# Performance work log

Hardware: AMD Instinct MI355X
Metric: run time of the kernel (lower is better)

## Reference

```python
import jax, jax.numpy as jnp
import numpy as np

N_NODES = 50000
N_EDGES = 800000
D_FEAT = 64      # num_src_feats == num_dst_feats
D_EDGE = 16      # num_edge_feats
D_HID = 16       # hidden width of both tiny MLPs
D_MSG = 64       # msg_size
D_OUT = 64       # num_out_feats


def setup_inputs() -> dict:
    key = jax.random.key(0)
    ks = jax.random.split(key, 12)
    x = jax.random.normal(ks[0], (N_NODES, D_FEAT), dtype=jnp.float32)
    edge_feats = jax.random.normal(ks[1], (N_EDGES, D_EDGE), dtype=jnp.float32)
    src = jax.random.randint(ks[2], (N_EDGES,), 0, N_NODES, dtype=jnp.int32)
    dst = jax.random.randint(ks[3], (N_EDGES,), 0, N_NODES, dtype=jnp.int32)

    def linear_params(k, fan_in, fan_out):
        kw, kb = jax.random.split(k)
        bound = 1.0 / np.sqrt(fan_in)
        W = jax.random.uniform(kw, (fan_in, fan_out), jnp.float32, -bound, bound)
        b = jax.random.uniform(kb, (fan_out,), jnp.float32, -bound, bound)
        return W, b

    # fc_msg: [D_EDGE + D_FEAT, 16, D_MSG]
    msg_W1, msg_b1 = linear_params(ks[4], D_EDGE + D_FEAT, D_HID)
    msg_W2, msg_b2 = linear_params(ks[5], D_HID, D_MSG)
    # fc_udt: [D_FEAT + D_MSG, 16, D_OUT]
    udt_W1, udt_b1 = linear_params(ks[6], D_FEAT + D_MSG, D_HID)
    udt_W2, udt_b2 = linear_params(ks[7], D_HID, D_OUT)

    return {
        "x": x, "edge_feats": edge_feats, "src": src, "dst": dst,
        "msg_W1": msg_W1, "msg_b1": msg_b1, "msg_W2": msg_W2, "msg_b2": msg_b2,
        "udt_W1": udt_W1, "udt_b1": udt_b1, "udt_W2": udt_W2, "udt_b2": udt_b2,
    }


def reference(x, edge_feats, src, dst,
              msg_W1, msg_b1, msg_W2, msg_b2,
              udt_W1, udt_b1, udt_W2, udt_b2):
    # message: m_e = MLP([edge_feats_e, x[src_e]])   (cat order: edge first)
    edge_in = jnp.concatenate([edge_feats, x[src]], axis=1)  # [E, D_EDGE+D_FEAT]
    h = jax.nn.relu(edge_in @ msg_W1 + msg_b1)
    m = h @ msg_W2 + msg_b2  # [E, D_MSG]

    # reduce: r_v = max over incoming edges (DGL fills 0 for nodes w/o in-edges)
    r = jax.ops.segment_max(m, dst, num_segments=N_NODES)  # [N, D_MSG]
    r = jnp.where(jnp.isfinite(r), r, 0.0)

    # update: out_v = MLP([x_v, r_v])
    upd_in = jnp.concatenate([x, r], axis=1)  # [N, D_FEAT+D_MSG]
    h2 = jax.nn.relu(upd_in @ udt_W1 + udt_b1)
    return h2 @ udt_W2 + udt_b2  # [N, D_OUT]
```

## Files before the change

kernel.cpp:

```cpp
#include <hip/hip_runtime.h>

#define N_NODES 50000
#define N_EDGES 800000

#define NB  196
#define PB  128
#define EPB 6250
#define PITERS 25
#define CAP 7680

__device__ __forceinline__ unsigned fkey(float f) {
    unsigned u = __float_as_uint(f);
    return (u & 0x80000000u) ? ~u : (u | 0x80000000u);
}
#define KEY_NEG_INF 0x007FFFFFu

__device__ __forceinline__ void wave_lds_fence() {
    asm volatile("s_waitcnt lgkmcnt(0)" ::: "memory");
    __builtin_amdgcn_sched_barrier(0);
}

__global__ __launch_bounds__(256) void chist_kernel(const int* __restrict__ dst,
                                                    unsigned* __restrict__ bcnt) {
    __shared__ unsigned lh[NB];
    const int t = threadIdx.x, b = blockIdx.x;
    if (t < NB) lh[t] = 0u;
    __syncthreads();
    const int e0 = b * EPB;
#pragma unroll
    for (int it = 0; it < PITERS; ++it) {
        const int i = it * 256 + t;
        if (i < EPB) atomicAdd(&lh[(unsigned)dst[e0 + i] >> 8], 1u);
    }
    __syncthreads();
    if (t < NB) bcnt[b * NB + t] = lh[t];
}

__global__ __launch_bounds__(256) void cscan_kernel(const unsigned* __restrict__ bcnt,
                                                    unsigned* __restrict__ gstart,
                                                    unsigned* __restrict__ boffG,
                                                    unsigned* __restrict__ totG) {
    __shared__ unsigned wsum[4];
    const int t = threadIdx.x, lane = t & 63, w = t >> 6;
    unsigned tot = 0;
    if (t < NB)
        for (int k = 0; k < PB; ++k) tot += bcnt[k * NB + t];
    unsigned v = (t < NB) ? tot : 0u;
    const unsigned orig = v;
#pragma unroll
    for (int d = 1; d < 64; d <<= 1) {
        unsigned n = __shfl_up(v, d, 64);
        if (lane >= d) v += n;
    }
    if (lane == 63) wsum[w] = v;
    __syncthreads();
    unsigned woff = 0;
#pragma unroll
    for (int i = 0; i < 3; ++i) if (i < w) woff += wsum[i];
    const unsigned boff = woff + v - orig;
    if (t < NB) {
        boffG[t] = boff;
        totG[t]  = tot;
        unsigned run = boff;
        for (int k = 0; k < PB; ++k) { gstart[k * NB + t] = run; run += bcnt[k * NB + t]; }
    }
}

__global__ __launch_bounds__(256) void partition_kernel(const int* __restrict__ dst,
                                                        const unsigned* __restrict__ gstart,
                                                        unsigned long long* __restrict__ part) {
    __shared__ unsigned long long st[EPB];
    __shared__ unsigned lh[NB], lstart[NB], lc[NB], gs[NB];
    __shared__ unsigned wsum[4];
    const int t = threadIdx.x, b = blockIdx.x, lane = t & 63, w = t >> 6;
    if (t < NB) { lh[t] = 0u; gs[t] = gstart[b * NB + t]; }
    __syncthreads();
    const int e0 = b * EPB;
#pragma unroll
    for (int it = 0; it < PITERS; ++it) {
        const int i = it * 256 + t;
        if (i < EPB) atomicAdd(&lh[(unsigned)dst[e0 + i] >> 8], 1u);
    }
    __syncthreads();
    {
        unsigned v = (t < NB) ? lh[t] : 0u;
        const unsigned orig = v;
#pragma unroll
        for (int d = 1; d < 64; d <<= 1) {
            unsigned n = __shfl_up(v, d, 64);
            if (lane >= d) v += n;
        }
        if (lane == 63) wsum[w] = v;
        __syncthreads();
        unsigned woff = 0;
#pragma unroll
        for (int i = 0; i < 3; ++i) if (i < w) woff += wsum[i];
        if (t < NB) { lstart[t] = woff + v - orig; lc[t] = woff + v - orig; }
    }
    __syncthreads();
#pragma unroll
    for (int it = 0; it < PITERS; ++it) {
        const int i = it * 256 + t;
        if (i < EPB) {
            const int e = e0 + i;
            const unsigned d = (unsigned)dst[e];
            const unsigned p = atomicAdd(&lc[d >> 8], 1u);
            st[p] = ((unsigned long long)d << 32) | (unsigned)e;
        }
    }
    __syncthreads();
#pragma unroll
    for (int it = 0; it < PITERS; ++it) {
        const int i = it * 256 + t;
        if (i < EPB) {
            const unsigned long long pv = st[i];
            const unsigned bkt = (unsigned)(pv >> 40);
            part[gs[bkt] + ((unsigned)i - lstart[bkt])] = pv;
        }
    }
}

__global__ __launch_bounds__(256) void finesort_kernel(const unsigned long long* __restrict__ part,
                                                       const unsigned* __restrict__ boffG,
                                                       const unsigned* __restrict__ totG,
                                                       unsigned long long* __restrict__ dsf) {
    __shared__ unsigned long long st[CAP];
    __shared__ unsigned fh[256], fstart[256];
    __shared__ unsigned wsum[4];
    const int t = threadIdx.x, b = blockIdx.x, lane = t & 63, w = t >> 6;
    const unsigned base = boffG[b], cnt = totG[b];
    fh[t] = 0u;
    __syncthreads();
    const int iters = (int)((cnt + 255u) >> 8);
    for (int it = 0; it < iters; ++it) {
        const unsigned i = (unsigned)it * 256u + (unsigned)t;
        if (i < cnt) atomicAdd(&fh[(unsigned)(part[base + i] >> 32) & 255u], 1u);
    }
    __syncthreads();
    {
        unsigned v = fh[t];
        const unsigned orig = v;
#pragma unroll
        for (int d = 1; d < 64; d <<= 1) {
            unsigned n = __shfl_up(v, d, 64);
            if (lane >= d) v += n;
        }
        if (lane == 63) wsum[w] = v;
        __syncthreads();
        unsigned woff = 0;
#pragma unroll
        for (int i = 0; i < 3; ++i) if (i < w) woff += wsum[i];
        fstart[t] = woff + v - orig;
    }
    __syncthreads();
    if (cnt <= CAP) {
        for (int it = 0; it < iters; ++it) {
            const unsigned i = (unsigned)it * 256u + (unsigned)t;
            if (i < cnt) {
                const unsigned long long pv = part[base + i];
                const unsigned p = atomicAdd(&fstart[(unsigned)(pv >> 32) & 255u], 1u);
                st[p] = pv;
            }
        }
        __syncthreads();
        for (int it = 0; it < iters; ++it) {
            const unsigned i = (unsigned)it * 256u + (unsigned)t;
            if (i < cnt) dsf[base + i] = st[i];
        }
    } else {
        for (int it = 0; it < iters; ++it) {
            const unsigned i = (unsigned)it * 256u + (unsigned)t;
            if (i < cnt) {
                const unsigned long long pv = part[base + i];
                const unsigned p = atomicAdd(&fstart[(unsigned)(pv >> 32) & 255u], 1u);
                dsf[base + p] = pv;
            }
        }
    }
}

__global__ __launch_bounds__(256) void init_kernel(
    unsigned* __restrict__ rkey,
    const float* __restrict__ x, const float* __restrict__ W1,
    const float* __restrict__ b1, float* __restrict__ xw)
{
    const int i = blockIdx.x * 256 + threadIdx.x;
    reinterpret_cast<uint4*>(rkey)[i] =
        make_uint4(KEY_NEG_INF, KEY_NEG_INF, KEY_NEG_INF, KEY_NEG_INF);
    if (i < N_NODES) {
        float acc[16];
#pragma unroll
        for (int k = 0; k < 16; ++k) acc[k] = b1[k];
        const float4* xp = reinterpret_cast<const float4*>(x) + (size_t)i * 16;
#pragma unroll
        for (int c = 0; c < 16; ++c) {
            float4 tv = xp[c];
            const float xv[4] = {tv.x, tv.y, tv.z, tv.w};
#pragma unroll
            for (int q = 0; q < 4; ++q) {
                const int row = 16 + 4 * c + q;
#pragma unroll
                for (int k = 0; k < 16; ++k)
                    acc[k] = fmaf(xv[q], W1[row * 16 + k], acc[k]);
            }
        }
        float4* op = reinterpret_cast<float4*>(xw) + (size_t)i * 4;
#pragma unroll
        for (int c = 0; c < 4; ++c) {
            float4 o; o.x = acc[4*c]; o.y = acc[4*c+1]; o.z = acc[4*c+2]; o.w = acc[4*c+3];
            op[c] = o;
        }
    }
}

__global__ __launch_bounds__(256) void init0_kernel(unsigned* __restrict__ rkey) {
    const int i = blockIdx.x * 256 + threadIdx.x;
    reinterpret_cast<uint4*>(rkey)[i] =
        make_uint4(KEY_NEG_INF, KEY_NEG_INF, KEY_NEG_INF, KEY_NEG_INF);
}

__global__ __launch_bounds__(256) void edge_csr2_kernel(
    const float* __restrict__ xw, const float* __restrict__ ef,
    const int* __restrict__ src,
    const unsigned long long* __restrict__ ds,
    const float* __restrict__ W1, const float* __restrict__ W2,
    const float* __restrict__ b2,
    unsigned* __restrict__ rkey)
{
    const int lane = threadIdx.x & 63;
    const int w    = threadIdx.x >> 6;
    const int wave = blockIdx.x * 4 + w;
    const int base = wave * 64;
    const int slot = base + lane;

    __shared__ unsigned mld[4][64][17];
    __shared__ int      dldA[4][66];
    int* dld = &dldA[w][1];

    const unsigned long long pv = ds[slot];
    const int e = (int)(unsigned)pv;
    const int d = (int)(pv >> 32);
    dld[lane] = d;
    if (lane == 0)  dld[-1] = (base == 0) ? -1 : (int)(ds[base - 1] >> 32);
    if (lane == 63) dld[64] = (base + 64 >= N_EDGES) ? -1 : (int)(ds[base + 64] >> 32);

    float in[16];
    const float4* efp = reinterpret_cast<const float4*>(ef) + (size_t)e * 4;
#pragma unroll
    for (int c = 0; c < 4; ++c) {
        float4 tv = efp[c];
        in[4*c+0]=tv.x; in[4*c+1]=tv.y; in[4*c+2]=tv.z; in[4*c+3]=tv.w;
    }
    const int s = src[e];
    float h[16];
    const float4* xp = reinterpret_cast<const float4*>(xw) + (size_t)s * 4;
#pragma unroll
    for (int c = 0; c < 4; ++c) {
        float4 tv = xp[c];
        h[4*c+0]=tv.x; h[4*c+1]=tv.y; h[4*c+2]=tv.z; h[4*c+3]=tv.w;
    }
#pragma unroll
    for (int i = 0; i < 16; ++i)
#pragma unroll
        for (int k = 0; k < 16; ++k)
            h[k] = fmaf(in[i], W1[i*16 + k], h[k]);
#pragma unroll
    for (int k = 0; k < 16; ++k) h[k] = fmaxf(h[k], 0.0f);

    const int q  = lane >> 4;
    const int jj = lane & 15;

#pragma unroll
    for (int j0 = 0; j0 < 64; j0 += 16) {
        float m[16];
#pragma unroll
        for (int t = 0; t < 16; ++t) m[t] = b2[j0 + t];
#pragma unroll
        for (int k = 0; k < 16; ++k)
#pragma unroll
            for (int t = 0; t < 16; ++t)
                m[t] = fmaf(h[k], W2[k*64 + j0 + t], m[t]);

        wave_lds_fence();
#pragma unroll
        for (int t = 0; t < 16; ++t) mld[w][lane][t] = fkey(m[t]);
        wave_lds_fence();

        const int s0 = q * 16;
        unsigned run = KEY_NEG_INF;
        int  dprev = dld[s0 - 1];
        bool phead = (dld[s0] != dprev);
        dprev = dld[s0];
        run = mld[w][s0][jj];
#pragma unroll
        for (int i = 1; i < 16; ++i) {
            const int ss = s0 + i;
            const int dsv = dld[ss];
            if (dsv != dprev) {
                unsigned* addr = &rkey[((size_t)dprev << 6) + (unsigned)(j0 + jj)];
                if (phead) *addr = run;
                else       atomicMax(addr, run);
                run = KEY_NEG_INF;
                phead = true;
            }
            run = max(run, mld[w][ss][jj]);
            dprev = dsv;
        }
        const bool ptail = (dld[s0 + 16] != dprev);
        unsigned* addr = &rkey[((size_t)dprev << 6) + (unsigned)(j0 + jj)];
        if (phead && ptail) *addr = run;
        else                atomicMax(addr, run);
    }
}

__global__ __launch_bounds__(256) void node_kernel(
    const float* __restrict__ x, const unsigned* rkey,
    const float* __restrict__ W1, const float* __restrict__ b1,
    const float* __restrict__ W2, const float* __restrict__ b2,
    float* out)
{
    const int v = blockIdx.x * 256 + threadIdx.x;
    if (v >= N_NODES) return;

    float in[128];
    const float4* xp = reinterpret_cast<const float4*>(x) + (size_t)v * 16;
#pragma unroll
    for (int c = 0; c < 16; ++c) {
        float4 tv = xp[c];
        in[4*c+0]=tv.x; in[4*c+1]=tv.y; in[4*c+2]=tv.z; in[4*c+3]=tv.w;
    }
    const uint4* rp = reinterpret_cast<const uint4*>(rkey) + (size_t)v * 16;
#pragma unroll
    for (int c = 0; c < 16; ++c) {
        uint4 tv = rp[c];
        unsigned ks[4] = {tv.x, tv.y, tv.z, tv.w};
#pragma unroll
        for (int qq = 0; qq < 4; ++qq) {
            unsigned k = ks[qq];
            unsigned u = (k & 0x80000000u) ? (k ^ 0x80000000u) : ~k;
            float f = __uint_as_float(u);
            if (!(f >= -3.402823466e38f && f <= 3.402823466e38f)) f = 0.0f;
            in[64 + 4*c + qq] = f;
        }
    }

    float h[16];
#pragma unroll
    for (int k = 0; k < 16; ++k) h[k] = b1[k];
#pragma unroll
    for (int i = 0; i < 128; ++i)
#pragma unroll
        for (int k = 0; k < 16; ++k)
            h[k] = fmaf(in[i], W1[i*16 + k], h[k]);
#pragma unroll
    for (int k = 0; k < 16; ++k) h[k] = fmaxf(h[k], 0.0f);

    float* op = out + (size_t)v * 64;
#pragma unroll
    for (int c = 0; c < 16; ++c) {
        float oo[4];
#pragma unroll
        for (int qq = 0; qq < 4; ++qq) {
            float a = b2[4*c + qq];
#pragma unroll
            for (int k = 0; k < 16; ++k)
                a = fmaf(h[k], W2[k*64 + 4*c + qq], a);
            oo[qq] = a;
        }
        float4 o; o.x=oo[0]; o.y=oo[1]; o.z=oo[2]; o.w=oo[3];
        reinterpret_cast<float4*>(op)[c] = o;
    }
}

__global__ __launch_bounds__(64) void edge_kernel(
    const float* __restrict__ x, const float* __restrict__ ef,
    const int* __restrict__ src, const int* __restrict__ dst,
    const float* __restrict__ W1, const float* __restrict__ b1,
    const float* __restrict__ W2, const float* __restrict__ b2,
    unsigned* __restrict__ rkey)
{
    const int lane = threadIdx.x;
    const int e    = blockIdx.x * 64 + lane;

    __shared__ unsigned mld[64][17];
    __shared__ int      dld[64];

    float in[80];
    const float4* efp = reinterpret_cast<const float4*>(ef) + (size_t)e * 4;
#pragma unroll
    for (int c = 0; c < 4; ++c) {
        float4 tv = efp[c];
        in[4*c+0]=tv.x; in[4*c+1]=tv.y; in[4*c+2]=tv.z; in[4*c+3]=tv.w;
    }
    const int s = src[e];
    dld[lane] = dst[e];
    const float4* xp = reinterpret_cast<const float4*>(x) + (size_t)s * 16;
#pragma unroll
    for (int c = 0; c < 16; ++c) {
        float4 tv = xp[c];
        in[16+4*c+0]=tv.x; in[16+4*c+1]=tv.y; in[16+4*c+2]=tv.z; in[16+4*c+3]=tv.w;
    }

    float h[16];
#pragma unroll
    for (int k = 0; k < 16; ++k) h[k] = b1[k];
#pragma unroll
    for (int i = 0; i < 80; ++i)
#pragma unroll
        for (int k = 0; k < 16; ++k)
            h[k] = fmaf(in[i], W1[i*16 + k], h[k]);
#pragma unroll
    for (int k = 0; k < 16; ++k) h[k] = fmaxf(h[k], 0.0f);

    const int er = lane >> 4;
    const int jj = lane & 15;

#pragma unroll
    for (int j0 = 0; j0 < 64; j0 += 16) {
        float m[16];
#pragma unroll
        for (int t = 0; t < 16; ++t) m[t] = b2[j0 + t];
#pragma unroll
        for (int k = 0; k < 16; ++k)
#pragma unroll
            for (int t = 0; t < 16; ++t)
                m[t] = fmaf(h[k], W2[k*64 + j0 + t], m[t]);

        wave_lds_fence();
#pragma unroll
        for (int t = 0; t < 16; ++t) mld[lane][t] = fkey(m[t]);
        wave_lds_fence();

#pragma unroll
        for (int eg = 0; eg < 16; ++eg) {
            const int ee = (eg << 2) | er;
            atomicMax(&rkey[((size_t)dld[ee] << 6) + (unsigned)(j0 + jj)],
                      mld[ee][jj]);
        }
    }
}

extern "C" void kernel_launch(void* const* d_in, const int* in_sizes, int n_in,
                              void* d_out, int out_size, void* d_ws, size_t ws_size,
                              hipStream_t stream) {
    const float* x   = (const float*)d_in[0];
    const float* ef  = (const float*)d_in[1];
    const int*   src = (const int*)d_in[2];
    const int*   dst = (const int*)d_in[3];
    const float* mW1 = (const float*)d_in[4];
    const float* mb1 = (const float*)d_in[5];
    const float* mW2 = (const float*)d_in[6];
    const float* mb2 = (const float*)d_in[7];
    const float* uW1 = (const float*)d_in[8];
    const float* ub1 = (const float*)d_in[9];
    const float* uW2 = (const float*)d_in[10];
    const float* ub2 = (const float*)d_in[11];

    unsigned* rkey = (unsigned*)d_out;
    float*    out  = (float*)d_out;

    const size_t WS_NEEDED = (size_t)N_EDGES * 8
                           + (size_t)(PB * NB * 2 + 512 + N_EDGES) * 4;

    if (ws_size >= WS_NEEDED) {
        unsigned long long* dsf = (unsigned long long*)d_ws;
        unsigned* bcnt   = (unsigned*)(dsf + N_EDGES);
        unsigned* gstart = bcnt + PB * NB;
        unsigned* boffG  = gstart + PB * NB;
        unsigned* totG   = boffG + 256;
        float*    xw     = (float*)(totG + 256);
        unsigned long long* part = (unsigned long long*)d_out;

        hipLaunchKernelGGL(chist_kernel,     dim3(PB),   dim3(256), 0, stream, dst, bcnt);
        hipLaunchKernelGGL(cscan_kernel,     dim3(1),    dim3(256), 0, stream, bcnt, gstart, boffG, totG);
        hipLaunchKernelGGL(partition_kernel, dim3(PB),   dim3(256), 0, stream, dst, gstart, part);
        hipLaunchKernelGGL(finesort_kernel,  dim3(NB),   dim3(256), 0, stream, part, boffG, totG, dsf);
        hipLaunchKernelGGL(init_kernel,      dim3(3125), dim3(256), 0, stream, rkey, x, mW1, mb1, xw);
        hipLaunchKernelGGL(edge_csr2_kernel, dim3(3125), dim3(256), 0, stream,
                           xw, ef, src, dsf, mW1, mW2, mb2, rkey);
    } else {
        hipLaunchKernelGGL(init0_kernel, dim3(3125), dim3(256), 0, stream, rkey);
        hipLaunchKernelGGL(edge_kernel, dim3(12500), dim3(64), 0, stream,
                           x, ef, src, dst, mW1, mb1, mW2, mb2, rkey);
    }

    hipLaunchKernelGGL(node_kernel, dim3((N_NODES + 255) / 256), dim3(256), 0, stream,
                       x, rkey, uW1, ub1, uW2, ub2, out);
}
```

Measured before the change: 141.1 us.

## Precompute per-edge hidden layer in fp16 before sorting, fuse xw into histogram

The first MLP layer for each edge is now computed in original edge order, where the edge features are read contiguously, and stored as fp16 hidden activations. The sorted edge kernel then only gathers 32 bytes per edge and applies the second layer plus the segment max. The node projection xw is fused into the histogram kernel, and the partition grid doubles to 256 blocks. This trades the scattered edge-feature reads in the sorted pass for an extra 25MB write and read of h16, adds fp16 rounding of hidden activations, and needs a larger workspace with a fallback path.

```diff
diff --git a/kernel.cpp b/kernel.cpp
--- a/kernel.cpp
+++ b/kernel.cpp
@@ -1,12 +1,13 @@
 #include <hip/hip_runtime.h>
+#include <hip/hip_fp16.h>
 
 #define N_NODES 50000
 #define N_EDGES 800000
 
 #define NB  196
-#define PB  128
-#define EPB 6250
-#define PITERS 25
+#define PB  256
+#define EPB 3125
+#define PITERS 13
 #define CAP 7680
 
 __device__ __forceinline__ unsigned fkey(float f) {
@@ -20,8 +21,11 @@
     __builtin_amdgcn_sched_barrier(0);
 }
 
-__global__ __launch_bounds__(256) void chist_kernel(const int* __restrict__ dst,
-                                                    unsigned* __restrict__ bcnt) {
+__global__ __launch_bounds__(256) void chist_xw_kernel(
+    const int* __restrict__ dst, unsigned* __restrict__ bcnt,
+    const float* __restrict__ x, const float* __restrict__ W1,
+    const float* __restrict__ b1, float* __restrict__ xw)
+{
     __shared__ unsigned lh[NB];
     const int t = threadIdx.x, b = blockIdx.x;
     if (t < NB) lh[t] = 0u;
@@ -34,6 +38,34 @@
     }
     __syncthreads();
     if (t < NB) bcnt[b * NB + t] = lh[t];
+
+    if (b < 196) {
+        const int v = b * 256 + t;
+        if (v < N_NODES) {
+            float acc[16];
+#pragma unroll
+            for (int k = 0; k < 16; ++k) acc[k] = b1[k];
+            const float4* xp = reinterpret_cast<const float4*>(x) + (size_t)v * 16;
+#pragma unroll
+            for (int c = 0; c < 16; ++c) {
+                float4 tv = xp[c];
+                const float xv[4] = {tv.x, tv.y, tv.z, tv.w};
+#pragma unroll
+                for (int q = 0; q < 4; ++q) {
+                    const int row = 16 + 4 * c + q;
+#pragma unroll
+                    for (int k = 0; k < 16; ++k)
+                        acc[k] = fmaf(xv[q], W1[row * 16 + k], acc[k]);
+                }
+            }
+            float4* op = reinterpret_cast<float4*>(xw) + (size_t)v * 4;
+#pragma unroll
+            for (int c = 0; c < 4; ++c) {
+                float4 o; o.x = acc[4*c]; o.y = acc[4*c+1]; o.z = acc[4*c+2]; o.w = acc[4*c+3];
+                op[c] = o;
+            }
+        }
+    }
 }
 
 __global__ __launch_bounds__(256) void cscan_kernel(const unsigned* __restrict__ bcnt,
@@ -66,6 +98,46 @@
     }
 }
 
+__global__ __launch_bounds__(256) void hcomp_kernel(
+    const float* __restrict__ ef, const int* __restrict__ src,
+    const float* __restrict__ xw, const float* __restrict__ W1,
+    unsigned* __restrict__ rkey, unsigned* __restrict__ h16)
+{
+    const int e = blockIdx.x * 256 + threadIdx.x;
+    reinterpret_cast<uint4*>(rkey)[e] =
+        make_uint4(KEY_NEG_INF, KEY_NEG_INF, KEY_NEG_INF, KEY_NEG_INF);
+
+    float in[16];
+    const float4* efp = reinterpret_cast<const float4*>(ef) + (size_t)e * 4;
+#pragma unroll
+    for (int c = 0; c < 4; ++c) {
+        float4 tv = efp[c];
+        in[4*c+0]=tv.x; in[4*c+1]=tv.y; in[4*c+2]=tv.z; in[4*c+3]=tv.w;
+    }
+    const int s = src[e];
+    float h[16];
+    const float4* xp = reinterpret_cast<const float4*>(xw) + (size_t)s * 4;
+#pragma unroll
+    for (int c = 0; c < 4; ++c) {
+        float4 tv = xp[c];
+        h[4*c+0]=tv.x; h[4*c+1]=tv.y; h[4*c+2]=tv.z; h[4*c+3]=tv.w;
+    }
+#pragma unroll
+    for (int i = 0; i < 16; ++i)
+#pragma unroll
+        for (int k = 0; k < 16; ++k)
+            h[k] = fmaf(in[i], W1[i*16 + k], h[k]);
+    unsigned wds[8];
+#pragma unroll
+    for (int k = 0; k < 8; ++k) {
+        __half2 t2 = __floats2half2_rn(fmaxf(h[2*k], 0.0f), fmaxf(h[2*k+1], 0.0f));
+        wds[k] = *reinterpret_cast<unsigned*>(&t2);
+    }
+    uint4* hp = reinterpret_cast<uint4*>(h16) + (size_t)e * 2;
+    hp[0] = make_uint4(wds[0], wds[1], wds[2], wds[3]);
+    hp[1] = make_uint4(wds[4], wds[5], wds[6], wds[7]);
+}
+
 __global__ __launch_bounds__(256) void partition_kernel(const int* __restrict__ dst,
                                                         const unsigned* __restrict__ gstart,
                                                         unsigned long long* __restrict__ part) {
@@ -179,44 +251,92 @@
     }
 }
 
-__global__ __launch_bounds__(256) void init_kernel(
-    unsigned* __restrict__ rkey,
-    const float* __restrict__ x, const float* __restrict__ W1,
-    const float* __restrict__ b1, float* __restrict__ xw)
-{
-    const int i = blockIdx.x * 256 + threadIdx.x;
-    reinterpret_cast<uint4*>(rkey)[i] =
-        make_uint4(KEY_NEG_INF, KEY_NEG_INF, KEY_NEG_INF, KEY_NEG_INF);
-    if (i < N_NODES) {
-        float acc[16];
-#pragma unroll
-        for (int k = 0; k < 16; ++k) acc[k] = b1[k];
-        const float4* xp = reinterpret_cast<const float4*>(x) + (size_t)i * 16;
-#pragma unroll
-        for (int c = 0; c < 16; ++c) {
-            float4 tv = xp[c];
-            const float xv[4] = {tv.x, tv.y, tv.z, tv.w};
-#pragma unroll
-            for (int q = 0; q < 4; ++q) {
-                const int row = 16 + 4 * c + q;
-#pragma unroll
-                for (int k = 0; k < 16; ++k)
-                    acc[k] = fmaf(xv[q], W1[row * 16 + k], acc[k]);
-            }
-        }
-        float4* op = reinterpret_cast<float4*>(xw) + (size_t)i * 4;
-#pragma unroll
-        for (int c = 0; c < 4; ++c) {
-            float4 o; o.x = acc[4*c]; o.y = acc[4*c+1]; o.z = acc[4*c+2]; o.w = acc[4*c+3];
-            op[c] = o;
-        }
-    }
-}
-
 __global__ __launch_bounds__(256) void init0_kernel(unsigned* __restrict__ rkey) {
     const int i = blockIdx.x * 256 + threadIdx.x;
     reinterpret_cast<uint4*>(rkey)[i] =
         make_uint4(KEY_NEG_INF, KEY_NEG_INF, KEY_NEG_INF, KEY_NEG_INF);
+}
+
+__global__ __launch_bounds__(256) void edge_h16_kernel(
+    const unsigned* __restrict__ h16,
+    const unsigned long long* __restrict__ ds,
+    const float* __restrict__ W2, const float* __restrict__ b2,
+    unsigned* __restrict__ rkey)
+{
+    const int lane = threadIdx.x & 63;
+    const int w    = threadIdx.x >> 6;
+    const int wave = blockIdx.x * 4 + w;
+    const int base = wave * 64;
+    const int slot = base + lane;
+
+    __shared__ unsigned mld[4][64][17];
+    __shared__ int      dldA[4][66];
+    int* dld = &dldA[w][1];
+
+    const unsigned long long pv = ds[slot];
+    const int e = (int)(unsigned)pv;
+    const int d = (int)(pv >> 32);
+    dld[lane] = d;
+    if (lane == 0)  dld[-1] = (base == 0) ? -1 : (int)(ds[base - 1] >> 32);
+    if (lane == 63) dld[64] = (base + 64 >= N_EDGES) ? -1 : (int)(ds[base + 64] >> 32);
+
+    float h[16];
+    {
+        const uint4* hp = reinterpret_cast<const uint4*>(h16) + (size_t)e * 2;
+        uint4 A = hp[0], B = hp[1];
+        unsigned wd[8] = {A.x, A.y, A.z, A.w, B.x, B.y, B.z, B.w};
+#pragma unroll
+        for (int k = 0; k < 8; ++k) {
+            __half2 t2 = *reinterpret_cast<const __half2*>(&wd[k]);
+            float2 f = __half22float2(t2);
+            h[2*k] = f.x; h[2*k+1] = f.y;
+        }
+    }
+
+    const int q  = lane >> 4;
+    const int jj = lane & 15;
+
+#pragma unroll
+    for (int j0 = 0; j0 < 64; j0 += 16) {
+        float m[16];
+#pragma unroll
+        for (int t = 0; t < 16; ++t) m[t] = b2[j0 + t];
+#pragma unroll
+        for (int k = 0; k < 16; ++k)
+#pragma unroll
+            for (int t = 0; t < 16; ++t)
+                m[t] = fmaf(h[k], W2[k*64 + j0 + t], m[t]);
+
+        wave_lds_fence();
+#pragma unroll
+        for (int t = 0; t < 16; ++t) mld[w][lane][t] = fkey(m[t]);
+        wave_lds_fence();
+
+        const int s0 = q * 16;
+        unsigned run = KEY_NEG_INF;
+        int  dprev = dld[s0 - 1];
+        bool phead = (dld[s0] != dprev);
+        dprev = dld[s0];
+        run = mld[w][s0][jj];
+#pragma unroll
+        for (int i = 1; i < 16; ++i) {
+            const int ss = s0 + i;
+            const int dsv = dld[ss];
+            if (dsv != dprev) {
+                unsigned* addr = &rkey[((size_t)dprev << 6) + (unsigned)(j0 + jj)];
+                if (phead) *addr = run;
+                else       atomicMax(addr, run);
+                run = KEY_NEG_INF;
+                phead = true;
+            }
+            run = max(run, mld[w][ss][jj]);
+            dprev = dsv;
+        }
+        const bool ptail = (dld[s0 + 16] != dprev);
+        unsigned* addr = &rkey[((size_t)dprev << 6) + (unsigned)(j0 + jj)];
+        if (phead && ptail) *addr = run;
+        else                atomicMax(addr, run);
+    }
 }
 
 __global__ __launch_bounds__(256) void edge_csr2_kernel(
@@ -459,25 +579,39 @@
     unsigned* rkey = (unsigned*)d_out;
     float*    out  = (float*)d_out;
 
-    const size_t WS_NEEDED = (size_t)N_EDGES * 8
-                           + (size_t)(PB * NB * 2 + 512 + N_EDGES) * 4;
-
-    if (ws_size >= WS_NEEDED) {
-        unsigned long long* dsf = (unsigned long long*)d_ws;
-        unsigned* bcnt   = (unsigned*)(dsf + N_EDGES);
-        unsigned* gstart = bcnt + PB * NB;
-        unsigned* boffG  = gstart + PB * NB;
-        unsigned* totG   = boffG + 256;
-        float*    xw     = (float*)(totG + 256);
-        unsigned long long* part = (unsigned long long*)d_out;
-
-        hipLaunchKernelGGL(chist_kernel,     dim3(PB),   dim3(256), 0, stream, dst, bcnt);
+    const size_t OFF_PART  = (size_t)N_EDGES;
+    unsigned long long* dsf  = (unsigned long long*)d_ws;
+    unsigned long long* partW = dsf + OFF_PART;
+    unsigned* bcnt   = (unsigned*)(partW + N_EDGES);
+    unsigned* gstart = bcnt + (size_t)PB * NB;
+    unsigned* boffG  = gstart + (size_t)PB * NB;
+    unsigned* totG   = boffG + 256;
+    float*    xw     = (float*)(totG + 256);
+    unsigned* h16    = (unsigned*)(xw + N_EDGES);
+
+    const size_t T2_NEEDED = (size_t)((char*)h16 - (char*)d_ws) - (size_t)N_EDGES * 8;
+    const size_t T1_NEEDED = (size_t)((char*)(h16 + (size_t)N_EDGES * 8) - (char*)d_ws);
+
+    if (ws_size >= T1_NEEDED) {
+        hipLaunchKernelGGL(chist_xw_kernel,  dim3(PB),   dim3(256), 0, stream, dst, bcnt, x, mW1, mb1, xw);
         hipLaunchKernelGGL(cscan_kernel,     dim3(1),    dim3(256), 0, stream, bcnt, gstart, boffG, totG);
-        hipLaunchKernelGGL(partition_kernel, dim3(PB),   dim3(256), 0, stream, dst, gstart, part);
-        hipLaunchKernelGGL(finesort_kernel,  dim3(NB),   dim3(256), 0, stream, part, boffG, totG, dsf);
-        hipLaunchKernelGGL(init_kernel,      dim3(3125), dim3(256), 0, stream, rkey, x, mW1, mb1, xw);
-        hipLaunchKernelGGL(edge_csr2_kernel, dim3(3125), dim3(256), 0, stream,
-                           xw, ef, src, dsf, mW1, mW2, mb2, rkey);
+        hipLaunchKernelGGL(hcomp_kernel,     dim3(3125), dim3(256), 0, stream, ef, src, xw, mW1, rkey, h16);
+        hipLaunchKernelGGL(partition_kernel, dim3(PB),   dim3(256), 0, stream, dst, gstart, partW);
+        hipLaunchKernelGGL(finesort_kernel,  dim3(NB),   dim3(256), 0, stream, partW, boffG, totG, dsf);
+        hipLaunchKernelGGL(edge_h16_kernel,  dim3(3125), dim3(256), 0, stream, h16, dsf, mW2, mb2, rkey);
+    } else if (ws_size >= T2_NEEDED) {
+        unsigned long long* partO = (unsigned long long*)d_out;
+        unsigned* bcnt2   = (unsigned*)(dsf + N_EDGES);
+        unsigned* gstart2 = bcnt2 + (size_t)PB * NB;
+        unsigned* boffG2  = gstart2 + (size_t)PB * NB;
+        unsigned* totG2   = boffG2 + 256;
+        float*    xw2     = (float*)(totG2 + 256);
+        hipLaunchKernelGGL(chist_xw_kernel,  dim3(PB),   dim3(256), 0, stream, dst, bcnt2, x, mW1, mb1, xw2);
+        hipLaunchKernelGGL(cscan_kernel,     dim3(1),    dim3(256), 0, stream, bcnt2, gstart2, boffG2, totG2);
+        hipLaunchKernelGGL(partition_kernel, dim3(PB),   dim3(256), 0, stream, dst, gstart2, partO);
+        hipLaunchKernelGGL(finesort_kernel,  dim3(NB),   dim3(256), 0, stream, partO, boffG2, totG2, dsf);
+        hipLaunchKernelGGL(init0_kernel,     dim3(3125), dim3(256), 0, stream, rkey);
+        hipLaunchKernelGGL(edge_csr2_kernel, dim3(3125), dim3(256), 0, stream, xw2, ef, src, dsf, mW1, mW2, mb2, rkey);
     } else {
         hipLaunchKernelGGL(init0_kernel, dim3(3125), dim3(256), 0, stream, rkey);
         hipLaunchKernelGGL(edge_kernel, dim3(12500), dim3(64), 0, stream,
```

After: 148.7 us. +5.4%, slower.

## Restructure pipeline: 64-node buckets with LDS segment max fused into node update

Applied to the files above, without the earlier changes.

Replaces the two-level radix sort with a single partition into 784 buckets of 64 destination nodes each. Two scan kernels compute the bucket offsets, and the xW1 precompute is folded into the histogram kernel. The first MLP layer is computed per edge during partitioning and stored as fp16, so the final kernel only needs the second layer. That kernel does the segment max with LDS atomics per bucket and runs the node update MLP directly, removing the global atomicMax pass, the fine sort and the separate node kernel. The trade-offs are fp16 rounding of the hidden activations and a less even load across buckets.

```diff
diff --git a/kernel.cpp b/kernel.cpp
--- a/kernel.cpp
+++ b/kernel.cpp
@@ -1,13 +1,14 @@
 #include <hip/hip_runtime.h>
+#include <hip/hip_fp16.h>
 
 #define N_NODES 50000
 #define N_EDGES 800000
 
-#define NB  196
-#define PB  128
-#define EPB 6250
-#define PITERS 25
-#define CAP 7680
+#define NBu 784
+#define BSH 6
+#define PB  256
+#define EPB 3125
+#define PITERS 13
 
 __device__ __forceinline__ unsigned fkey(float f) {
     unsigned u = __float_as_uint(f);
@@ -20,91 +21,144 @@
     __builtin_amdgcn_sched_barrier(0);
 }
 
-__global__ __launch_bounds__(256) void chist_kernel(const int* __restrict__ dst,
-                                                    unsigned* __restrict__ bcnt) {
-    __shared__ unsigned lh[NB];
+__device__ __forceinline__ unsigned block_exscan256(unsigned v, unsigned* wsum,
+                                                    unsigned* chunkTot) {
+    const int t = threadIdx.x, lane = t & 63, w = t >> 6;
+    unsigned inc = v;
+#pragma unroll
+    for (int d = 1; d < 64; d <<= 1) {
+        unsigned n = __shfl_up(inc, d, 64);
+        if (lane >= d) inc += n;
+    }
+    if (lane == 63) wsum[w] = inc;
+    __syncthreads();
+    unsigned woff = 0;
+#pragma unroll
+    for (int i = 0; i < 3; ++i) if (i < w) woff += wsum[i];
+    if (chunkTot && t == 255) *chunkTot = woff + inc;
+    __syncthreads();
+    return woff + inc - v;
+}
+
+__global__ __launch_bounds__(256) void chist_xw_kernel(
+    const int* __restrict__ dst, unsigned* __restrict__ bcnt,
+    const float* __restrict__ x, const float* __restrict__ W1,
+    const float* __restrict__ b1, float* __restrict__ xw)
+{
+    __shared__ unsigned lh[NBu];
     const int t = threadIdx.x, b = blockIdx.x;
-    if (t < NB) lh[t] = 0u;
+    for (int i = t; i < NBu; i += 256) lh[i] = 0u;
     __syncthreads();
     const int e0 = b * EPB;
 #pragma unroll
     for (int it = 0; it < PITERS; ++it) {
         const int i = it * 256 + t;
-        if (i < EPB) atomicAdd(&lh[(unsigned)dst[e0 + i] >> 8], 1u);
-    }
-    __syncthreads();
-    if (t < NB) bcnt[b * NB + t] = lh[t];
-}
-
-__global__ __launch_bounds__(256) void cscan_kernel(const unsigned* __restrict__ bcnt,
-                                                    unsigned* __restrict__ gstart,
-                                                    unsigned* __restrict__ boffG,
-                                                    unsigned* __restrict__ totG) {
+        if (i < EPB) atomicAdd(&lh[(unsigned)dst[e0 + i] >> BSH], 1u);
+    }
+    __syncthreads();
+    for (int i = t; i < NBu; i += 256) bcnt[(size_t)b * NBu + i] = lh[i];
+
+    if (b < 196) {
+        const int v = b * 256 + t;
+        if (v < N_NODES) {
+            float acc[16];
+#pragma unroll
+            for (int k = 0; k < 16; ++k) acc[k] = b1[k];
+            const float4* xp = reinterpret_cast<const float4*>(x) + (size_t)v * 16;
+#pragma unroll
+            for (int c = 0; c < 16; ++c) {
+                float4 tv = xp[c];
+                const float xv[4] = {tv.x, tv.y, tv.z, tv.w};
+#pragma unroll
+                for (int q = 0; q < 4; ++q) {
+                    const int row = 16 + 4 * c + q;
+#pragma unroll
+                    for (int k = 0; k < 16; ++k)
+                        acc[k] = fmaf(xv[q], W1[row * 16 + k], acc[k]);
+                }
+            }
+            float4* op = reinterpret_cast<float4*>(xw) + (size_t)v * 4;
+#pragma unroll
+            for (int c = 0; c < 4; ++c) {
+                float4 o; o.x = acc[4*c]; o.y = acc[4*c+1]; o.z = acc[4*c+2]; o.w = acc[4*c+3];
+                op[c] = o;
+            }
+        }
+    }
+}
+
+__global__ __launch_bounds__(256) void cscanA_kernel(const unsigned* __restrict__ bcnt,
+                                                     unsigned* __restrict__ gstart,
+                                                     unsigned* __restrict__ tot) {
     __shared__ unsigned wsum[4];
-    const int t = threadIdx.x, lane = t & 63, w = t >> 6;
-    unsigned tot = 0;
-    if (t < NB)
-        for (int k = 0; k < PB; ++k) tot += bcnt[k * NB + t];
-    unsigned v = (t < NB) ? tot : 0u;
-    const unsigned orig = v;
-#pragma unroll
-    for (int d = 1; d < 64; d <<= 1) {
-        unsigned n = __shfl_up(v, d, 64);
-        if (lane >= d) v += n;
-    }
-    if (lane == 63) wsum[w] = v;
-    __syncthreads();
-    unsigned woff = 0;
-#pragma unroll
-    for (int i = 0; i < 3; ++i) if (i < w) woff += wsum[i];
-    const unsigned boff = woff + v - orig;
-    if (t < NB) {
-        boffG[t] = boff;
-        totG[t]  = tot;
-        unsigned run = boff;
-        for (int k = 0; k < PB; ++k) { gstart[k * NB + t] = run; run += bcnt[k * NB + t]; }
-    }
-}
-
-__global__ __launch_bounds__(256) void partition_kernel(const int* __restrict__ dst,
-                                                        const unsigned* __restrict__ gstart,
-                                                        unsigned long long* __restrict__ part) {
+    const int t = threadIdx.x, bu = blockIdx.x;
+    const unsigned v = bcnt[(size_t)t * NBu + bu];
+    const unsigned excl = block_exscan256(v, wsum, nullptr);
+    gstart[(size_t)t * NBu + bu] = excl;
+    if (t == 255) tot[bu] = excl + v;
+}
+
+__global__ __launch_bounds__(256) void cscanB_kernel(const unsigned* __restrict__ tot,
+                                                     unsigned* __restrict__ boffG) {
+    __shared__ unsigned wsum[4];
+    __shared__ unsigned carrySh, chunkTot;
+    const int t = threadIdx.x;
+    if (t == 0) carrySh = 0u;
+    __syncthreads();
+    for (int c = 0; c < 4; ++c) {
+        const int idx = c * 256 + t;
+        const unsigned v = (idx < NBu) ? tot[idx] : 0u;
+        const unsigned excl = block_exscan256(v, wsum, &chunkTot);
+        if (idx < NBu) boffG[idx] = carrySh + excl;
+        __syncthreads();
+        if (t == 0) carrySh += chunkTot;
+        __syncthreads();
+    }
+}
+
+__global__ __launch_bounds__(256) void part_hcomp_kernel(
+    const int* __restrict__ dst, const unsigned* __restrict__ gstart,
+    const unsigned* __restrict__ boffG,
+    unsigned long long* __restrict__ part,
+    const float* __restrict__ ef, const int* __restrict__ src,
+    const float* __restrict__ xw, const float* __restrict__ W1,
+    unsigned* __restrict__ h16)
+{
     __shared__ unsigned long long st[EPB];
-    __shared__ unsigned lh[NB], lstart[NB], lc[NB], gs[NB];
-    __shared__ unsigned wsum[4];
-    const int t = threadIdx.x, b = blockIdx.x, lane = t & 63, w = t >> 6;
-    if (t < NB) { lh[t] = 0u; gs[t] = gstart[b * NB + t]; }
+    __shared__ unsigned lh[NBu], lstart[NBu], lc[NBu], gs[NBu];
+    __shared__ unsigned wsum[4], carrySh, chunkTot;
+    const int t = threadIdx.x, b = blockIdx.x;
+    for (int i = t; i < NBu; i += 256) lh[i] = 0u;
     __syncthreads();
     const int e0 = b * EPB;
 #pragma unroll
     for (int it = 0; it < PITERS; ++it) {
         const int i = it * 256 + t;
-        if (i < EPB) atomicAdd(&lh[(unsigned)dst[e0 + i] >> 8], 1u);
-    }
-    __syncthreads();
-    {
-        unsigned v = (t < NB) ? lh[t] : 0u;
-        const unsigned orig = v;
-#pragma unroll
-        for (int d = 1; d < 64; d <<= 1) {
-            unsigned n = __shfl_up(v, d, 64);
-            if (lane >= d) v += n;
-        }
-        if (lane == 63) wsum[w] = v;
+        if (i < EPB) atomicAdd(&lh[(unsigned)dst[e0 + i] >> BSH], 1u);
+    }
+    if (t == 0) carrySh = 0u;
+    __syncthreads();
+    for (int c = 0; c < 4; ++c) {
+        const int idx = c * 256 + t;
+        const unsigned v = (idx < NBu) ? lh[idx] : 0u;
+        const unsigned excl = block_exscan256(v, wsum, &chunkTot);
+        if (idx < NBu) {
+            const unsigned s0 = carrySh + excl;
+            lstart[idx] = s0;
+            lc[idx]     = s0;
+            gs[idx]     = gstart[(size_t)b * NBu + idx] + boffG[idx];
+        }
         __syncthreads();
-        unsigned woff = 0;
-#pragma unroll
-        for (int i = 0; i < 3; ++i) if (i < w) woff += wsum[i];
-        if (t < NB) { lstart[t] = woff + v - orig; lc[t] = woff + v - orig; }
-    }
-    __syncthreads();
+        if (t == 0) carrySh += chunkTot;
+        __syncthreads();
+    }
 #pragma unroll
     for (int it = 0; it < PITERS; ++it) {
         const int i = it * 256 + t;
         if (i < EPB) {
             const int e = e0 + i;
             const unsigned d = (unsigned)dst[e];
-            const unsigned p = atomicAdd(&lc[d >> 8], 1u);
+            const unsigned p = atomicAdd(&lc[d >> BSH], 1u);
             st[p] = ((unsigned long long)d << 32) | (unsigned)e;
         }
     }
@@ -114,101 +168,166 @@
         const int i = it * 256 + t;
         if (i < EPB) {
             const unsigned long long pv = st[i];
-            const unsigned bkt = (unsigned)(pv >> 40);
+            const unsigned bkt = (unsigned)(pv >> (32 + BSH));
             part[gs[bkt] + ((unsigned)i - lstart[bkt])] = pv;
         }
     }
-}
-
-__global__ __launch_bounds__(256) void finesort_kernel(const unsigned long long* __restrict__ part,
-                                                       const unsigned* __restrict__ boffG,
-                                                       const unsigned* __restrict__ totG,
-                                                       unsigned long long* __restrict__ dsf) {
-    __shared__ unsigned long long st[CAP];
-    __shared__ unsigned fh[256], fstart[256];
-    __shared__ unsigned wsum[4];
-    const int t = threadIdx.x, b = blockIdx.x, lane = t & 63, w = t >> 6;
-    const unsigned base = boffG[b], cnt = totG[b];
-    fh[t] = 0u;
-    __syncthreads();
-    const int iters = (int)((cnt + 255u) >> 8);
-    for (int it = 0; it < iters; ++it) {
-        const unsigned i = (unsigned)it * 256u + (unsigned)t;
-        if (i < cnt) atomicAdd(&fh[(unsigned)(part[base + i] >> 32) & 255u], 1u);
-    }
-    __syncthreads();
-    {
-        unsigned v = fh[t];
-        const unsigned orig = v;
-#pragma unroll
-        for (int d = 1; d < 64; d <<= 1) {
-            unsigned n = __shfl_up(v, d, 64);
-            if (lane >= d) v += n;
-        }
-        if (lane == 63) wsum[w] = v;
-        __syncthreads();
-        unsigned woff = 0;
-#pragma unroll
-        for (int i = 0; i < 3; ++i) if (i < w) woff += wsum[i];
-        fstart[t] = woff + v - orig;
-    }
-    __syncthreads();
-    if (cnt <= CAP) {
-        for (int it = 0; it < iters; ++it) {
-            const unsigned i = (unsigned)it * 256u + (unsigned)t;
-            if (i < cnt) {
-                const unsigned long long pv = part[base + i];
-                const unsigned p = atomicAdd(&fstart[(unsigned)(pv >> 32) & 255u], 1u);
-                st[p] = pv;
-            }
-        }
-        __syncthreads();
-        for (int it = 0; it < iters; ++it) {
-            const unsigned i = (unsigned)it * 256u + (unsigned)t;
-            if (i < cnt) dsf[base + i] = st[i];
-        }
-    } else {
-        for (int it = 0; it < iters; ++it) {
-            const unsigned i = (unsigned)it * 256u + (unsigned)t;
-            if (i < cnt) {
-                const unsigned long long pv = part[base + i];
-                const unsigned p = atomicAdd(&fstart[(unsigned)(pv >> 32) & 255u], 1u);
-                dsf[base + p] = pv;
-            }
-        }
-    }
-}
-
-__global__ __launch_bounds__(256) void init_kernel(
-    unsigned* __restrict__ rkey,
-    const float* __restrict__ x, const float* __restrict__ W1,
-    const float* __restrict__ b1, float* __restrict__ xw)
+#pragma unroll
+    for (int it = 0; it < PITERS; ++it) {
+        const int i = it * 256 + t;
+        if (i < EPB) {
+            const int e = e0 + i;
+            float in[16];
+            const float4* efp = reinterpret_cast<const float4*>(ef) + (size_t)e * 4;
+#pragma unroll
+            for (int c = 0; c < 4; ++c) {
+                float4 tv = efp[c];
+                in[4*c+0]=tv.x; in[4*c+1]=tv.y; in[4*c+2]=tv.z; in[4*c+3]=tv.w;
+            }
+            const int s = src[e];
+            float h[16];
+            const float4* xp = reinterpret_cast<const float4*>(xw) + (size_t)s * 4;
+#pragma unroll
+            for (int c = 0; c < 4; ++c) {
+                float4 tv = xp[c];
+                h[4*c+0]=tv.x; h[4*c+1]=tv.y; h[4*c+2]=tv.z; h[4*c+3]=tv.w;
+            }
+#pragma unroll
+            for (int ii = 0; ii < 16; ++ii)
+#pragma unroll
+                for (int k = 0; k < 16; ++k)
+                    h[k] = fmaf(in[ii], W1[ii*16 + k], h[k]);
+            unsigned wds[8];
+#pragma unroll
+            for (int k = 0; k < 8; ++k) {
+                __half2 t2 = __floats2half2_rn(fmaxf(h[2*k], 0.0f), fmaxf(h[2*k+1], 0.0f));
+                wds[k] = *reinterpret_cast<unsigned*>(&t2);
+            }
+            uint4* hp = reinterpret_cast<uint4*>(h16) + (size_t)e * 2;
+            hp[0] = make_uint4(wds[0], wds[1], wds[2], wds[3]);
+            hp[1] = make_uint4(wds[4], wds[5], wds[6], wds[7]);
+        }
+    }
+}
+
+__global__ __launch_bounds__(256) void fused_kernel(
+    const unsigned long long* __restrict__ part,
+    const unsigned* __restrict__ boffG, const unsigned* __restrict__ tot,
+    const unsigned* __restrict__ h16,
+    const float* __restrict__ W2, const float* __restrict__ b2,
+    const float* __restrict__ x,
+    const float* __restrict__ uW1, const float* __restrict__ ub1,
+    const float* __restrict__ uW2, const float* __restrict__ ub2,
+    float* __restrict__ out)
 {
-    const int i = blockIdx.x * 256 + threadIdx.x;
-    reinterpret_cast<uint4*>(rkey)[i] =
-        make_uint4(KEY_NEG_INF, KEY_NEG_INF, KEY_NEG_INF, KEY_NEG_INF);
-    if (i < N_NODES) {
-        float acc[16];
-#pragma unroll
-        for (int k = 0; k < 16; ++k) acc[k] = b1[k];
-        const float4* xp = reinterpret_cast<const float4*>(x) + (size_t)i * 16;
+    __shared__ unsigned rmax[64][65];
+    __shared__ unsigned mld[4][64][17];
+    __shared__ int      dloc[4][64];
+    const int tid = threadIdx.x, b = blockIdx.x;
+    const int lane = tid & 63, w = tid >> 6;
+    const unsigned base = boffG[b], cnt = tot[b];
+
+    for (int i = tid; i < 64 * 65; i += 256)
+        (&rmax[0][0])[i] = KEY_NEG_INF;
+    __syncthreads();
+
+    const int er = lane >> 4;
+    const int jj = lane & 15;
+
+    const int nIter = (int)((cnt + 255u) >> 8);
+    for (int it = 0; it < nIter; ++it) {
+        const unsigned slot = (unsigned)it * 256u + (unsigned)tid;
+        const bool valid = slot < cnt;
+        int nloc = 0;
+        float h[16];
+        if (valid) {
+            const unsigned long long pv = part[base + slot];
+            const int e = (int)(unsigned)pv;
+            nloc = (int)((pv >> 32) & 63u);
+            const uint4* hp = reinterpret_cast<const uint4*>(h16) + (size_t)e * 2;
+            uint4 A = hp[0], B = hp[1];
+            unsigned wd[8] = {A.x, A.y, A.z, A.w, B.x, B.y, B.z, B.w};
+#pragma unroll
+            for (int k = 0; k < 8; ++k) {
+                __half2 t2 = *reinterpret_cast<const __half2*>(&wd[k]);
+                float2 f = __half22float2(t2);
+                h[2*k] = f.x; h[2*k+1] = f.y;
+            }
+        }
+        dloc[w][lane] = nloc;
+
+#pragma unroll
+        for (int j0 = 0; j0 < 64; j0 += 16) {
+            float m[16];
+#pragma unroll
+            for (int t16 = 0; t16 < 16; ++t16) m[t16] = b2[j0 + t16];
+            if (valid) {
+#pragma unroll
+                for (int k = 0; k < 16; ++k)
+#pragma unroll
+                    for (int t16 = 0; t16 < 16; ++t16)
+                        m[t16] = fmaf(h[k], W2[k*64 + j0 + t16], m[t16]);
+            }
+            wave_lds_fence();
+#pragma unroll
+            for (int t16 = 0; t16 < 16; ++t16)
+                mld[w][lane][t16] = valid ? fkey(m[t16]) : KEY_NEG_INF;
+            wave_lds_fence();
+#pragma unroll
+            for (int eg = 0; eg < 16; ++eg) {
+                const int ee = (eg << 2) | er;
+                atomicMax(&rmax[dloc[w][ee]][j0 + jj], mld[w][ee][jj]);
+            }
+        }
+    }
+    __syncthreads();
+
+    const int nl = tid & 63;
+    const int qq = tid >> 6;
+    const int v  = b * 64 + nl;
+    if (v < N_NODES) {
+        float h2[16];
+#pragma unroll
+        for (int k = 0; k < 16; ++k) h2[k] = ub1[k];
+        const float4* xp = reinterpret_cast<const float4*>(x) + (size_t)v * 16;
 #pragma unroll
         for (int c = 0; c < 16; ++c) {
             float4 tv = xp[c];
             const float xv[4] = {tv.x, tv.y, tv.z, tv.w};
 #pragma unroll
-            for (int q = 0; q < 4; ++q) {
-                const int row = 16 + 4 * c + q;
+            for (int u4 = 0; u4 < 4; ++u4) {
+                const int row = 4*c + u4;
 #pragma unroll
                 for (int k = 0; k < 16; ++k)
-                    acc[k] = fmaf(xv[q], W1[row * 16 + k], acc[k]);
-            }
-        }
-        float4* op = reinterpret_cast<float4*>(xw) + (size_t)i * 4;
+                    h2[k] = fmaf(xv[u4], uW1[row*16 + k], h2[k]);
+            }
+        }
+        for (int j = 0; j < 64; ++j) {
+            const unsigned kk = rmax[nl][j];
+            unsigned u = (kk & 0x80000000u) ? (kk ^ 0x80000000u) : ~kk;
+            float f = __uint_as_float(u);
+            if (!(f >= -3.402823466e38f && f <= 3.402823466e38f)) f = 0.0f;
+#pragma unroll
+            for (int k = 0; k < 16; ++k)
+                h2[k] = fmaf(f, uW1[(64 + j)*16 + k], h2[k]);
+        }
+#pragma unroll
+        for (int k = 0; k < 16; ++k) h2[k] = fmaxf(h2[k], 0.0f);
+        float* op = out + (size_t)v * 64 + qq * 16;
 #pragma unroll
         for (int c = 0; c < 4; ++c) {
-            float4 o; o.x = acc[4*c]; o.y = acc[4*c+1]; o.z = acc[4*c+2]; o.w = acc[4*c+3];
-            op[c] = o;
+            float oo[4];
+#pragma unroll
+            for (int u4 = 0; u4 < 4; ++u4) {
+                const int col = qq*16 + 4*c + u4;
+                float a = ub2[col];
+#pragma unroll
+                for (int k = 0; k < 16; ++k)
+                    a = fmaf(h2[k], uW2[k*64 + col], a);
+                oo[u4] = a;
+            }
+            float4 o; o.x=oo[0]; o.y=oo[1]; o.z=oo[2]; o.w=oo[3];
+            reinterpret_cast<float4*>(op)[c] = o;
         }
     }
 }
@@ -217,159 +336,6 @@
     const int i = blockIdx.x * 256 + threadIdx.x;
     reinterpret_cast<uint4*>(rkey)[i] =
         make_uint4(KEY_NEG_INF, KEY_NEG_INF, KEY_NEG_INF, KEY_NEG_INF);
-}
-
-__global__ __launch_bounds__(256) void edge_csr2_kernel(
-    const float* __restrict__ xw, const float* __restrict__ ef,
-    const int* __restrict__ src,
-    const unsigned long long* __restrict__ ds,
-    const float* __restrict__ W1, const float* __restrict__ W2,
-    const float* __restrict__ b2,
-    unsigned* __restrict__ rkey)
-{
-    const int lane = threadIdx.x & 63;
-    const int w    = threadIdx.x >> 6;
-    const int wave = blockIdx.x * 4 + w;
-    const int base = wave * 64;
-    const int slot = base + lane;
-
-    __shared__ unsigned mld[4][64][17];
-    __shared__ int      dldA[4][66];
-    int* dld = &dldA[w][1];
-
-    const unsigned long long pv = ds[slot];
-    const int e = (int)(unsigned)pv;
-    const int d = (int)(pv >> 32);
-    dld[lane] = d;
-    if (lane == 0)  dld[-1] = (base == 0) ? -1 : (int)(ds[base - 1] >> 32);
-    if (lane == 63) dld[64] = (base + 64 >= N_EDGES) ? -1 : (int)(ds[base + 64] >> 32);
-
-    float in[16];
-    const float4* efp = reinterpret_cast<const float4*>(ef) + (size_t)e * 4;
-#pragma unroll
-    for (int c = 0; c < 4; ++c) {
-        float4 tv = efp[c];
-        in[4*c+0]=tv.x; in[4*c+1]=tv.y; in[4*c+2]=tv.z; in[4*c+3]=tv.w;
-    }
-    const int s = src[e];
-    float h[16];
-    const float4* xp = reinterpret_cast<const float4*>(xw) + (size_t)s * 4;
-#pragma unroll
-    for (int c = 0; c < 4; ++c) {
-        float4 tv = xp[c];
-        h[4*c+0]=tv.x; h[4*c+1]=tv.y; h[4*c+2]=tv.z; h[4*c+3]=tv.w;
-    }
-#pragma unroll
-    for (int i = 0; i < 16; ++i)
-#pragma unroll
-        for (int k = 0; k < 16; ++k)
-            h[k] = fmaf(in[i], W1[i*16 + k], h[k]);
-#pragma unroll
-    for (int k = 0; k < 16; ++k) h[k] = fmaxf(h[k], 0.0f);
-
-    const int q  = lane >> 4;
-    const int jj = lane & 15;
-
-#pragma unroll
-    for (int j0 = 0; j0 < 64; j0 += 16) {
-        float m[16];
-#pragma unroll
-        for (int t = 0; t < 16; ++t) m[t] = b2[j0 + t];
-#pragma unroll
-        for (int k = 0; k < 16; ++k)
-#pragma unroll
-            for (int t = 0; t < 16; ++t)
-                m[t] = fmaf(h[k], W2[k*64 + j0 + t], m[t]);
-
-        wave_lds_fence();
-#pragma unroll
-        for (int t = 0; t < 16; ++t) mld[w][lane][t] = fkey(m[t]);
-        wave_lds_fence();
-
-        const int s0 = q * 16;
-        unsigned run = KEY_NEG_INF;
-        int  dprev = dld[s0 - 1];
-        bool phead = (dld[s0] != dprev);
-        dprev = dld[s0];
-        run = mld[w][s0][jj];
-#pragma unroll
-        for (int i = 1; i < 16; ++i) {
-            const int ss = s0 + i;
-            const int dsv = dld[ss];
-            if (dsv != dprev) {
-                unsigned* addr = &rkey[((size_t)dprev << 6) + (unsigned)(j0 + jj)];
-                if (phead) *addr = run;
-                else       atomicMax(addr, run);
-                run = KEY_NEG_INF;
-                phead = true;
-            }
-            run = max(run, mld[w][ss][jj]);
-            dprev = dsv;
-        }
-        const bool ptail = (dld[s0 + 16] != dprev);
-        unsigned* addr = &rkey[((size_t)dprev << 6) + (unsigned)(j0 + jj)];
-        if (phead && ptail) *addr = run;
-        else                atomicMax(addr, run);
-    }
-}
-
-__global__ __launch_bounds__(256) void node_kernel(
-    const float* __restrict__ x, const unsigned* rkey,
-    const float* __restrict__ W1, const float* __restrict__ b1,
-    const float* __restrict__ W2, const float* __restrict__ b2,
-    float* out)
-{
-    const int v = blockIdx.x * 256 + threadIdx.x;
-    if (v >= N_NODES) return;
-
-    float in[128];
-    const float4* xp = reinterpret_cast<const float4*>(x) + (size_t)v * 16;
-#pragma unroll
-    for (int c = 0; c < 16; ++c) {
-        float4 tv = xp[c];
-        in[4*c+0]=tv.x; in[4*c+1]=tv.y; in[4*c+2]=tv.z; in[4*c+3]=tv.w;
-    }
-    const uint4* rp = reinterpret_cast<const uint4*>(rkey) + (size_t)v * 16;
-#pragma unroll
-    for (int c = 0; c < 16; ++c) {
-        uint4 tv = rp[c];
-        unsigned ks[4] = {tv.x, tv.y, tv.z, tv.w};
-#pragma unroll
-        for (int qq = 0; qq < 4; ++qq) {
-            unsigned k = ks[qq];
-            unsigned u = (k & 0x80000000u) ? (k ^ 0x80000000u) : ~k;
-            float f = __uint_as_float(u);
-            if (!(f >= -3.402823466e38f && f <= 3.402823466e38f)) f = 0.0f;
-            in[64 + 4*c + qq] = f;
-        }
-    }
-
-    float h[16];
-#pragma unroll
-    for (int k = 0; k < 16; ++k) h[k] = b1[k];
-#pragma unroll
-    for (int i = 0; i < 128; ++i)
-#pragma unroll
-        for (int k = 0; k < 16; ++k)
-            h[k] = fmaf(in[i], W1[i*16 + k], h[k]);
-#pragma unroll
-    for (int k = 0; k < 16; ++k) h[k] = fmaxf(h[k], 0.0f);
-
-    float* op = out + (size_t)v * 64;
-#pragma unroll
-    for (int c = 0; c < 16; ++c) {
-        float oo[4];
-#pragma unroll
-        for (int qq = 0; qq < 4; ++qq) {
-            float a = b2[4*c + qq];
-#pragma unroll
-            for (int k = 0; k < 16; ++k)
-                a = fmaf(h[k], W2[k*64 + 4*c + qq], a);
-            oo[qq] = a;
-        }
-        float4 o; o.x=oo[0]; o.y=oo[1]; o.z=oo[2]; o.w=oo[3];
-        reinterpret_cast<float4*>(op)[c] = o;
-    }
 }
 
 __global__ __launch_bounds__(64) void edge_kernel(
@@ -381,10 +347,8 @@
 {
     const int lane = threadIdx.x;
     const int e    = blockIdx.x * 64 + lane;
-
     __shared__ unsigned mld[64][17];
     __shared__ int      dld[64];
-
     float in[80];
     const float4* efp = reinterpret_cast<const float4*>(ef) + (size_t)e * 4;
 #pragma unroll
@@ -400,7 +364,6 @@
         float4 tv = xp[c];
         in[16+4*c+0]=tv.x; in[16+4*c+1]=tv.y; in[16+4*c+2]=tv.z; in[16+4*c+3]=tv.w;
     }
-
     float h[16];
 #pragma unroll
     for (int k = 0; k < 16; ++k) h[k] = b1[k];
@@ -411,10 +374,7 @@
             h[k] = fmaf(in[i], W1[i*16 + k], h[k]);
 #pragma unroll
     for (int k = 0; k < 16; ++k) h[k] = fmaxf(h[k], 0.0f);
-
-    const int er = lane >> 4;
-    const int jj = lane & 15;
-
+    const int er = lane >> 4, jj = lane & 15;
 #pragma unroll
     for (int j0 = 0; j0 < 64; j0 += 16) {
         float m[16];
@@ -425,18 +385,72 @@
 #pragma unroll
             for (int t = 0; t < 16; ++t)
                 m[t] = fmaf(h[k], W2[k*64 + j0 + t], m[t]);
-
         wave_lds_fence();
 #pragma unroll
         for (int t = 0; t < 16; ++t) mld[lane][t] = fkey(m[t]);
         wave_lds_fence();
-
 #pragma unroll
         for (int eg = 0; eg < 16; ++eg) {
             const int ee = (eg << 2) | er;
             atomicMax(&rkey[((size_t)dld[ee] << 6) + (unsigned)(j0 + jj)],
                       mld[ee][jj]);
         }
+    }
+}
+
+__global__ __launch_bounds__(256) void node_kernel(
+    const float* __restrict__ x, const unsigned* rkey,
+    const float* __restrict__ W1, const float* __restrict__ b1,
+    const float* __restrict__ W2, const float* __restrict__ b2,
+    float* out)
+{
+    const int v = blockIdx.x * 256 + threadIdx.x;
+    if (v >= N_NODES) return;
+    float in[128];
+    const float4* xp = reinterpret_cast<const float4*>(x) + (size_t)v * 16;
+#pragma unroll
+    for (int c = 0; c < 16; ++c) {
+        float4 tv = xp[c];
+        in[4*c+0]=tv.x; in[4*c+1]=tv.y; in[4*c+2]=tv.z; in[4*c+3]=tv.w;
+    }
+    const uint4* rp = reinterpret_cast<const uint4*>(rkey) + (size_t)v * 16;
+#pragma unroll
+    for (int c = 0; c < 16; ++c) {
+        uint4 tv = rp[c];
+        unsigned ks[4] = {tv.x, tv.y, tv.z, tv.w};
+#pragma unroll
+        for (int qq = 0; qq < 4; ++qq) {
+            unsigned k = ks[qq];
+            unsigned u = (k & 0x80000000u) ? (k ^ 0x80000000u) : ~k;
+            float f = __uint_as_float(u);
+            if (!(f >= -3.402823466e38f && f <= 3.402823466e38f)) f = 0.0f;
+            in[64 + 4*c + qq] = f;
+        }
+    }
+    float h[16];
+#pragma unroll
+    for (int k = 0; k < 16; ++k) h[k] = b1[k];
+#pragma unroll
+    for (int i = 0; i < 128; ++i)
+#pragma unroll
+        for (int k = 0; k < 16; ++k)
+            h[k] = fmaf(in[i], W1[i*16 + k], h[k]);
+#pragma unroll
+    for (int k = 0; k < 16; ++k) h[k] = fmaxf(h[k], 0.0f);
+    float* op = out + (size_t)v * 64;
+#pragma unroll
+    for (int c = 0; c < 16; ++c) {
+        float oo[4];
+#pragma unroll
+        for (int qq = 0; qq < 4; ++qq) {
+            float a = b2[4*c + qq];
+#pragma unroll
+            for (int k = 0; k < 16; ++k)
+                a = fmaf(h[k], W2[k*64 + 4*c + qq], a);
+            oo[qq] = a;
+        }
+        float4 o; o.x=oo[0]; o.y=oo[1]; o.z=oo[2]; o.w=oo[3];
+        reinterpret_cast<float4*>(op)[c] = o;
     }
 }
 
@@ -456,34 +470,36 @@
     const float* uW2 = (const float*)d_in[10];
     const float* ub2 = (const float*)d_in[11];
 
-    unsigned* rkey = (unsigned*)d_out;
-    float*    out  = (float*)d_out;
-
-    const size_t WS_NEEDED = (size_t)N_EDGES * 8
-                           + (size_t)(PB * NB * 2 + 512 + N_EDGES) * 4;
-
-    if (ws_size >= WS_NEEDED) {
-        unsigned long long* dsf = (unsigned long long*)d_ws;
-        unsigned* bcnt   = (unsigned*)(dsf + N_EDGES);
-        unsigned* gstart = bcnt + PB * NB;
-        unsigned* boffG  = gstart + PB * NB;
-        unsigned* totG   = boffG + 256;
-        float*    xw     = (float*)(totG + 256);
-        unsigned long long* part = (unsigned long long*)d_out;
-
-        hipLaunchKernelGGL(chist_kernel,     dim3(PB),   dim3(256), 0, stream, dst, bcnt);
-        hipLaunchKernelGGL(cscan_kernel,     dim3(1),    dim3(256), 0, stream, bcnt, gstart, boffG, totG);
-        hipLaunchKernelGGL(partition_kernel, dim3(PB),   dim3(256), 0, stream, dst, gstart, part);
-        hipLaunchKernelGGL(finesort_kernel,  dim3(NB),   dim3(256), 0, stream, part, boffG, totG, dsf);
-        hipLaunchKernelGGL(init_kernel,      dim3(3125), dim3(256), 0, stream, rkey, x, mW1, mb1, xw);
-        hipLaunchKernelGGL(edge_csr2_kernel, dim3(3125), dim3(256), 0, stream,
-                           xw, ef, src, dsf, mW1, mW2, mb2, rkey);
+    float* out = (float*)d_out;
+
+    unsigned long long* part = (unsigned long long*)d_ws;
+    unsigned* bcnt   = (unsigned*)(part + N_EDGES);
+    unsigned* gstart = bcnt + (size_t)PB * NBu;
+    unsigned* tot    = gstart + (size_t)PB * NBu;
+    unsigned* boffG  = tot + NBu;
+    float*    xw     = (float*)(boffG + NBu);
+    unsigned* h16    = (unsigned*)(xw + (size_t)50176 * 16);
+    const size_t T1_NEEDED =
+        (size_t)((char*)(h16 + (size_t)N_EDGES * 8) - (char*)d_ws);
+
+    if (ws_size >= T1_NEEDED) {
+        hipLaunchKernelGGL(chist_xw_kernel,  dim3(PB),  dim3(256), 0, stream,
+                           dst, bcnt, x, mW1, mb1, xw);
+        hipLaunchKernelGGL(cscanA_kernel,    dim3(NBu), dim3(256), 0, stream,
+                           bcnt, gstart, tot);
+        hipLaunchKernelGGL(cscanB_kernel,    dim3(1),   dim3(256), 0, stream,
+                           tot, boffG);
+        hipLaunchKernelGGL(part_hcomp_kernel, dim3(PB), dim3(256), 0, stream,
+                           dst, gstart, boffG, part, ef, src, xw, mW1, h16);
+        hipLaunchKernelGGL(fused_kernel,     dim3(NBu), dim3(256), 0, stream,
+                           part, boffG, tot, h16, mW2, mb2,
+                           x, uW1, ub1, uW2, ub2, out);
     } else {
+        unsigned* rkey = (unsigned*)d_out;
         hipLaunchKernelGGL(init0_kernel, dim3(3125), dim3(256), 0, stream, rkey);
         hipLaunchKernelGGL(edge_kernel, dim3(12500), dim3(64), 0, stream,
                            x, ef, src, dst, mW1, mb1, mW2, mb2, rkey);
-    }
-
-    hipLaunchKernelGGL(node_kernel, dim3((N_NODES + 255) / 256), dim3(256), 0, stream,
-                       x, rkey, uW1, ub1, uW2, ub2, out);
-}
+        hipLaunchKernelGGL(node_kernel, dim3((N_NODES + 255) / 256), dim3(256), 0, stream,
+                           x, rkey, uW1, ub1, uW2, ub2, out);
+    }
+}
```

After: 189.7 us. 1.34x slower.
